# Kernel optimization log

Measured on AMD Instinct MI355X. Metric: run time of the kernel, lower is better.

## Reference

```python
import jax, jax.numpy as jnp
import numpy as np

N, E, IN_DIM, OUT_DIM, SEM_DIM = 50000, 800000, 128, 128, 128
EPS = 1e-8


def setup_inputs() -> dict:
    key = jax.random.key(0)
    k = jax.random.split(key, 8)
    x = jax.random.normal(k[0], (N, IN_DIM), dtype=jnp.float32)
    edge_index = jax.random.randint(k[1], (2, E), 0, N, dtype=jnp.int64)
    semantic_vec = jax.random.normal(k[2], (N, SEM_DIM), dtype=jnp.float32)
    s = 1.0 / np.sqrt(IN_DIM)
    W_src = jax.random.uniform(k[3], (OUT_DIM, IN_DIM), jnp.float32, -s, s)
    b_src = jax.random.uniform(k[4], (OUT_DIM,), jnp.float32, -s, s)
    W_dst = jax.random.uniform(k[5], (OUT_DIM, IN_DIM), jnp.float32, -s, s)
    b_dst = jax.random.uniform(k[6], (OUT_DIM,), jnp.float32, -s, s)
    return {"x": x, "edge_index": edge_index, "semantic_vec": semantic_vec,
            "W_src": W_src, "b_src": b_src, "W_dst": W_dst, "b_dst": b_dst}


def _scatter_softmax(sim, dst, num_segments):
    # numerically stable segment-wise softmax over edges grouped by dst
    seg_max = jax.ops.segment_max(sim, dst, num_segments=num_segments)
    seg_max = jnp.where(jnp.isneginf(seg_max), 0.0, seg_max)
    e = jnp.exp(sim - seg_max[dst])
    seg_sum = jax.ops.segment_sum(e, dst, num_segments=num_segments)
    return e / (seg_sum[dst] + 1e-16)


def reference(x, edge_index, semantic_vec, W_src, b_src, W_dst, b_dst):
    src, dst = edge_index[0], edge_index[1]
    x_j = x[src] @ W_src.T + b_src           # [E, out_dim]
    # cosine similarity with torch eps semantics
    a = semantic_vec[src]
    b = semantic_vec[dst]
    na = jnp.maximum(jnp.linalg.norm(a, axis=-1), EPS)
    nb = jnp.maximum(jnp.linalg.norm(b, axis=-1), EPS)
    sim = jnp.sum(a * b, axis=-1) / (na * nb)  # [E]
    attn = _scatter_softmax(sim, dst, x.shape[0])
    msg = attn[:, None] * x_j                 # [E, out_dim]
    out = jax.ops.segment_sum(msg, dst, num_segments=x.shape[0])
    return out
```

## Files before the change

### kernel.cpp

```cpp
#include <hip/hip_runtime.h>
#include <hip/hip_fp16.h>

#define Nn 50000
#define Ee 800000
#define D  128
#define SLOT 64

#define B_SCAT 782
#define B_GEMM 782
#define B_NORM 3125

typedef _Float16 f16x8 __attribute__((ext_vector_type(8)));
typedef _Float16 h2    __attribute__((ext_vector_type(2)));
typedef float    f32x4 __attribute__((ext_vector_type(4)));


__global__ __launch_bounds__(256) void k_pre(const float* __restrict__ x,
                                             const float* __restrict__ W,
                                             const float* __restrict__ b,
                                             const int* __restrict__ ei,
                                             const float* __restrict__ sem,
                                             __half* __restrict__ blob,
                                             int* __restrict__ cnt,
                                             unsigned short* __restrict__ slot16) {
  __shared__ __half sW16[128 * 136] __attribute__((aligned(16)));
  int bid = blockIdx.x, tid = threadIdx.x;

  if (bid < B_SCAT) {
    int base = bid * 1024 + tid;
#pragma unroll
    for (int u = 0; u < 4; u++) {
      int e = base + u * 256;
      if (e < Ee) {
        int s = ei[e], d = ei[Ee + e];
        int pos = atomicAdd(cnt + d, 1);
        if (pos < SLOT)
          slot16[(size_t)d * SLOT + pos] = (unsigned short)s;
      }
    }
  } else if (bid < B_SCAT + B_GEMM) {
    int gb = bid - B_SCAT;
    int n0 = gb * 64;

    for (int r = 0; r < 16; r++) {
      int i = tid + 256 * r;
      int row = i >> 5, c4 = (i & 31) << 2;
      float4 w = *(const float4*)(W + (size_t)row * 128 + c4);
      __half2* dst = (__half2*)&sW16[row * 136 + c4];
      dst[0] = __floats2half2_rn(w.x, w.y);
      dst[1] = __floats2half2_rn(w.z, w.w);
    }

    int wave = tid >> 6, lane = tid & 63;
    int g = lane >> 4, n16 = lane & 15;
    int m0 = n0 + wave * 16;

    int arow = m0 + n16; if (arow >= Nn) arow = Nn - 1;
    const float* xr = x + (size_t)arow * 128 + g * 8;
    union { f16x8 v; __half2 h[4]; } af[4];
#pragma unroll
    for (int kt = 0; kt < 4; kt++) {
      float4 u = *(const float4*)(xr + kt * 32);
      float4 q = *(const float4*)(xr + kt * 32 + 4);
      af[kt].h[0] = __floats2half2_rn(u.x, u.y);
      af[kt].h[1] = __floats2half2_rn(u.z, u.w);
      af[kt].h[2] = __floats2half2_rn(q.x, q.y);
      af[kt].h[3] = __floats2half2_rn(q.z, q.w);
    }
    __syncthreads();

    f32x4 acc[8];
#pragma unroll
    for (int jt = 0; jt < 8; jt++) {
      float bias = b[jt * 16 + n16];
      acc[jt] = (f32x4){bias, bias, bias, bias};
    }
#pragma unroll
    for (int kt = 0; kt < 4; kt++) {
#pragma unroll
      for (int jt = 0; jt < 8; jt++) {
        f16x8 bf = *(const f16x8*)(&sW16[(jt * 16 + n16) * 136 + kt * 32 + g * 8]);
        acc[jt] = __builtin_amdgcn_mfma_f32_16x16x32_f16(af[kt].v, bf, acc[jt], 0, 0, 0);
      }
    }
#pragma unroll
    for (int jt = 0; jt < 8; jt++) {
#pragma unroll
      for (int r = 0; r < 4; r++) {
        int row = m0 + g * 4 + r;
        if (row < Nn)
          blob[(size_t)row * 256 + 128 + jt * 16 + n16] = __float2half(acc[jt][r]);
      }
    }
  } else {
    int nb = (bid - B_SCAT - B_GEMM) * 16;
    int wave = tid >> 6, lane = tid & 63;
#pragma unroll
    for (int it = 0; it < 4; it++) {
      int n = nb + it * 4 + wave;
      const float2 v = *(const float2*)(sem + (size_t)n * D + 2 * lane);
      float p = v.x * v.x + v.y * v.y;
#pragma unroll
      for (int off = 32; off > 0; off >>= 1) p += __shfl_xor(p, off);
      float inv = 1.0f / fmaxf(sqrtf(p), 1e-8f);
      *(__half2*)(blob + (size_t)n * 256 + 2 * lane) = __floats2half2_rn(v.x * inv, v.y * inv);
    }
  }
}

__global__ __launch_bounds__(256) void k_fused(const __half* __restrict__ blob,
                                               const unsigned short* __restrict__ slot16,
                                               const int* __restrict__ cnt,
                                               float* __restrict__ out) {
  int d = (blockIdx.x * 256 + threadIdx.x) >> 6;
  int lane = threadIdx.x & 63;
  int g = lane >> 4, l16 = lane & 15;
  int c = cnt[d]; if (c > SLOT) c = SLOT;

  int sv = (lane < c) ? (int)slot16[(size_t)d * SLOT + lane] : 0;

  f16x8 dh = *(const f16x8*)(blob + (size_t)d * 256 + l16 * 8);

  float o[8] = {0, 0, 0, 0, 0, 0, 0, 0};
  float Sp = 0.0f;

  for (int i = 0; i < c; i += 4) {
    int e = i + g;
    int ce = e < c ? e : c - 1;
    int sa = __shfl(sv, ce);
    const __half* nbp = blob + (size_t)sa * 256;
    f16x8 rs = *(const f16x8*)(nbp + l16 * 8);
    f16x8 ry = *(const f16x8*)(nbp + 128 + l16 * 8);
    float p = __builtin_amdgcn_fdot2((h2){rs[0], rs[1]}, (h2){dh[0], dh[1]}, 0.0f, false);
    p = __builtin_amdgcn_fdot2((h2){rs[2], rs[3]}, (h2){dh[2], dh[3]}, p, false);
    p = __builtin_amdgcn_fdot2((h2){rs[4], rs[5]}, (h2){dh[4], dh[5]}, p, false);
    p = __builtin_amdgcn_fdot2((h2){rs[6], rs[7]}, (h2){dh[6], dh[7]}, p, false);
    p += __shfl_xor(p, 1); p += __shfl_xor(p, 2);
    p += __shfl_xor(p, 4); p += __shfl_xor(p, 8);
    float ew = __expf(p); if (e >= c) ew = 0.0f;
    Sp += ew;
#pragma unroll
    for (int k = 0; k < 8; k++) o[k] += ew * (float)ry[k];
  }

#pragma unroll
  for (int k = 0; k < 8; k++) {
    o[k] += __shfl_xor(o[k], 16);
    o[k] += __shfl_xor(o[k], 32);
  }
  Sp += __shfl_xor(Sp, 16);
  Sp += __shfl_xor(Sp, 32);

  if (g == 0) {
    float inv = 1.0f / (Sp + 1e-16f);
    float4 r0; r0.x = o[0] * inv; r0.y = o[1] * inv; r0.z = o[2] * inv; r0.w = o[3] * inv;
    float4 r1; r1.x = o[4] * inv; r1.y = o[5] * inv; r1.z = o[6] * inv; r1.w = o[7] * inv;
    float* op = out + (size_t)d * D + l16 * 8;
    *(float4*)op = r0;
    *(float4*)(op + 4) = r1;
  }
}

extern "C" void kernel_launch(void* const* d_in, const int* in_sizes, int n_in,
                              void* d_out, int out_size, void* d_ws, size_t ws_size,
                              hipStream_t stream) {
  const float* x     = (const float*)d_in[0];
  const int*   ei    = (const int*)d_in[1];
  const float* sem   = (const float*)d_in[2];
  const float* W_src = (const float*)d_in[3];
  const float* b_src = (const float*)d_in[4];
  float* out = (float*)d_out;

  char* ws = (char*)d_ws;
  const size_t O_BLOB = 0;
  const size_t O_CNT  = 25600000;
  const size_t O_SS   = 25804800;
  const size_t NEED   = 32204800;
  if (ws_size < NEED) return;

  __half* blob = (__half*)(ws + O_BLOB);
  int* cnt = (int*)(ws + O_CNT);
  unsigned short* slot16 = (unsigned short*)(ws + O_SS);

  hipMemsetAsync(cnt, 0, 50048 * sizeof(int), stream);
  k_pre<<<B_SCAT + B_GEMM + B_NORM, 256, 0, stream>>>(x, W_src, b_src, ei, sem,
                                                      blob, cnt, slot16);
  k_fused<<<(Nn + 3) / 4, 256, 0, stream>>>(blob, slot16, cnt, out);
}
```

Measured before the change: 216.8 us.

## Interleave pre-kernel roles per block and drop shared-memory weight staging in GEMM

```diff
diff --git a/kernel.cpp b/kernel.cpp
--- a/kernel.cpp
+++ b/kernel.cpp
@@ -6,28 +6,27 @@
 #define D  128
 #define SLOT 64
 
-#define B_SCAT 782
-#define B_GEMM 782
-#define B_NORM 3125
+#define NGRP 782
+#define GRID_PRE (NGRP * 7)
 
 typedef _Float16 f16x8 __attribute__((ext_vector_type(8)));
 typedef _Float16 h2    __attribute__((ext_vector_type(2)));
 typedef float    f32x4 __attribute__((ext_vector_type(4)));
 
 
-__global__ __launch_bounds__(256) void k_pre(const float* __restrict__ x,
-                                             const float* __restrict__ W,
-                                             const float* __restrict__ b,
-                                             const int* __restrict__ ei,
-                                             const float* __restrict__ sem,
-                                             __half* __restrict__ blob,
-                                             int* __restrict__ cnt,
-                                             unsigned short* __restrict__ slot16) {
-  __shared__ __half sW16[128 * 136] __attribute__((aligned(16)));
+__global__ __launch_bounds__(256, 8) void k_pre(const float* __restrict__ x,
+                                                const float* __restrict__ W,
+                                                const float* __restrict__ b,
+                                                const int* __restrict__ ei,
+                                                const float* __restrict__ sem,
+                                                __half* __restrict__ blob,
+                                                int* __restrict__ cnt,
+                                                unsigned short* __restrict__ slot16) {
   int bid = blockIdx.x, tid = threadIdx.x;
+  int nb = bid / 7, r = bid % 7;
 
-  if (bid < B_SCAT) {
-    int base = bid * 1024 + tid;
+  if (r == 0) {
+    int base = nb * 1024 + tid;
 #pragma unroll
     for (int u = 0; u < 4; u++) {
       int e = base + u * 256;
@@ -38,72 +37,74 @@
           slot16[(size_t)d * SLOT + pos] = (unsigned short)s;
       }
     }
-  } else if (bid < B_SCAT + B_GEMM) {
-    int gb = bid - B_SCAT;
-    int n0 = gb * 64;
+  } else if (r <= 2) {
+    int gb = nb * 2 + (r - 1);
+    int n0 = gb * 32;
+    int wave = tid >> 6, lane = tid & 63;
+    int rs = (wave >> 1) * 16;
+    int ch = (wave & 1) * 64;
+    int g = lane >> 4, n16 = lane & 15;
 
-    for (int r = 0; r < 16; r++) {
-      int i = tid + 256 * r;
-      int row = i >> 5, c4 = (i & 31) << 2;
-      float4 w = *(const float4*)(W + (size_t)row * 128 + c4);
-      __half2* dst = (__half2*)&sW16[row * 136 + c4];
-      dst[0] = __floats2half2_rn(w.x, w.y);
-      dst[1] = __floats2half2_rn(w.z, w.w);
-    }
-
-    int wave = tid >> 6, lane = tid & 63;
-    int g = lane >> 4, n16 = lane & 15;
-    int m0 = n0 + wave * 16;
-
-    int arow = m0 + n16; if (arow >= Nn) arow = Nn - 1;
+    int arow = n0 + rs + n16; if (arow >= Nn) arow = Nn - 1;
     const float* xr = x + (size_t)arow * 128 + g * 8;
     union { f16x8 v; __half2 h[4]; } af[4];
 #pragma unroll
     for (int kt = 0; kt < 4; kt++) {
-      float4 u = *(const float4*)(xr + kt * 32);
-      float4 q = *(const float4*)(xr + kt * 32 + 4);
-      af[kt].h[0] = __floats2half2_rn(u.x, u.y);
-      af[kt].h[1] = __floats2half2_rn(u.z, u.w);
-      af[kt].h[2] = __floats2half2_rn(q.x, q.y);
-      af[kt].h[3] = __floats2half2_rn(q.z, q.w);
+      float4 u0 = *(const float4*)(xr + kt * 32);
+      float4 u1 = *(const float4*)(xr + kt * 32 + 4);
+      af[kt].h[0] = __floats2half2_rn(u0.x, u0.y);
+      af[kt].h[1] = __floats2half2_rn(u0.z, u0.w);
+      af[kt].h[2] = __floats2half2_rn(u1.x, u1.y);
+      af[kt].h[3] = __floats2half2_rn(u1.z, u1.w);
     }
-    __syncthreads();
 
-    f32x4 acc[8];
+    f32x4 acc[4];
 #pragma unroll
-    for (int jt = 0; jt < 8; jt++) {
-      float bias = b[jt * 16 + n16];
+    for (int jt = 0; jt < 4; jt++) {
+      float bias = b[ch + jt * 16 + n16];
       acc[jt] = (f32x4){bias, bias, bias, bias};
     }
+
+    const float* wr = W + (size_t)(ch + n16) * 128 + g * 8;
 #pragma unroll
     for (int kt = 0; kt < 4; kt++) {
 #pragma unroll
-      for (int jt = 0; jt < 8; jt++) {
-        f16x8 bf = *(const f16x8*)(&sW16[(jt * 16 + n16) * 136 + kt * 32 + g * 8]);
-        acc[jt] = __builtin_amdgcn_mfma_f32_16x16x32_f16(af[kt].v, bf, acc[jt], 0, 0, 0);
+      for (int jt = 0; jt < 4; jt++) {
+        const float* wp = wr + (size_t)jt * 16 * 128 + kt * 32;
+        float4 w0 = *(const float4*)(wp);
+        float4 w1 = *(const float4*)(wp + 4);
+        union { f16x8 v; __half2 h[4]; } bf;
+        bf.h[0] = __floats2half2_rn(w0.x, w0.y);
+        bf.h[1] = __floats2half2_rn(w0.z, w0.w);
+        bf.h[2] = __floats2half2_rn(w1.x, w1.y);
+        bf.h[3] = __floats2half2_rn(w1.z, w1.w);
+        acc[jt] = __builtin_amdgcn_mfma_f32_16x16x32_f16(af[kt].v, bf.v, acc[jt], 0, 0, 0);
       }
     }
 #pragma unroll
-    for (int jt = 0; jt < 8; jt++) {
+    for (int jt = 0; jt < 4; jt++) {
 #pragma unroll
-      for (int r = 0; r < 4; r++) {
-        int row = m0 + g * 4 + r;
+      for (int rr = 0; rr < 4; rr++) {
+        int row = n0 + rs + g * 4 + rr;
         if (row < Nn)
-          blob[(size_t)row * 256 + 128 + jt * 16 + n16] = __float2half(acc[jt][r]);
+          blob[(size_t)row * 256 + 128 + ch + jt * 16 + n16] = __float2half(acc[jt][rr]);
       }
     }
   } else {
-    int nb = (bid - B_SCAT - B_GEMM) * 16;
+    int idx = nb * 4 + (r - 3);
+    int nb16 = idx * 16;
     int wave = tid >> 6, lane = tid & 63;
 #pragma unroll
     for (int it = 0; it < 4; it++) {
-      int n = nb + it * 4 + wave;
-      const float2 v = *(const float2*)(sem + (size_t)n * D + 2 * lane);
-      float p = v.x * v.x + v.y * v.y;
+      int n = nb16 + it * 4 + wave;
+      if (n < Nn) {
+        const float2 v = *(const float2*)(sem + (size_t)n * D + 2 * lane);
+        float p = v.x * v.x + v.y * v.y;
 #pragma unroll
-      for (int off = 32; off > 0; off >>= 1) p += __shfl_xor(p, off);
-      float inv = 1.0f / fmaxf(sqrtf(p), 1e-8f);
-      *(__half2*)(blob + (size_t)n * 256 + 2 * lane) = __floats2half2_rn(v.x * inv, v.y * inv);
+        for (int off = 32; off > 0; off >>= 1) p += __shfl_xor(p, off);
+        float inv = 1.0f / fmaxf(sqrtf(p), 1e-8f);
+        *(__half2*)(blob + (size_t)n * 256 + 2 * lane) = __floats2half2_rn(v.x * inv, v.y * inv);
+      }
     }
   }
 }
@@ -183,7 +184,6 @@
   unsigned short* slot16 = (unsigned short*)(ws + O_SS);
 
   hipMemsetAsync(cnt, 0, 50048 * sizeof(int), stream);
-  k_pre<<<B_SCAT + B_GEMM + B_NORM, 256, 0, stream>>>(x, W_src, b_src, ei, sem,
-                                                      blob, cnt, slot16);
+  k_pre<<<GRID_PRE, 256, 0, stream>>>(x, W_src, b_src, ei, sem, blob, cnt, slot16);
   k_fused<<<(Nn + 3) / 4, 256, 0, stream>>>(blob, slot16, cnt, out);
 }
```

New measurement: 228.6 us. 5.5% more time.
